# Performance work log

Measured on AMD Instinct MI355X. Metric: run time of the kernel, lower is better.

Reference implementation:

```python
import jax, jax.numpy as jnp
import numpy as np
import math

B, S, D, H = 4, 1024, 512, 8
DK = D // H
NEG = -1e32


def setup_inputs() -> dict:
    key = jax.random.key(0)
    ks = jax.random.split(key, 16)
    f = lambda k, shape: jax.random.normal(k, shape, dtype=jnp.float32)
    w = 1.0 / math.sqrt(D)  # xavier-ish scale
    return {
        'query_mean': f(ks[0], (B, S, D)),
        'query_cov': f(ks[1], (B, S, D)),
        'key_mean': f(ks[2], (B, S, D)),
        'key_cov': f(ks[3], (B, S, D)),
        'values_mean': f(ks[4], (B, S, D)),
        'values_cov': f(ks[5], (B, S, D)),
        'Wk_mean': f(ks[6], (D, D)) * w, 'bk_mean': jnp.zeros((D,), jnp.float32),
        'Wk_cov': f(ks[7], (D, D)) * w, 'bk_cov': jnp.zeros((D,), jnp.float32),
        'Wv_mean': f(ks[8], (D, D)) * w, 'bv_mean': jnp.zeros((D,), jnp.float32),
        'Wv_cov': f(ks[9], (D, D)) * w, 'bv_cov': jnp.zeros((D,), jnp.float32),
        'Wo_mean': f(ks[10], (D, D)) * w, 'bo_mean': jnp.zeros((D,), jnp.float32),
        'Wo_cov': f(ks[11], (D, D)) * w, 'bo_cov': jnp.zeros((D,), jnp.float32),
        'gammas': f(ks[12], (H, 1, 1)) * 0.1,
        'mask': jnp.tril(jnp.ones((1, 1, S, S), dtype=jnp.int32)),
    }


def _forward(query_mean, query_cov, key_mean, key_cov, values_mean, values_cov,
             Wk_mean, bk_mean, Wk_cov, bk_cov, Wv_mean, bv_mean, Wv_cov, bv_cov,
             Wo_mean, bo_mean, Wo_cov, bo_cov, gammas, mask):
    def heads(x, W, b):  # [B,S,D] -> [B,H,S,DK]
        return (x @ W + b).reshape(B, S, H, DK).transpose(0, 2, 1, 3)

    # kq_same=True: queries and keys share the k linears
    qm = heads(query_mean, Wk_mean, bk_mean)
    qc = heads(query_cov, Wk_cov, bk_cov)
    km = heads(key_mean, Wk_mean, bk_mean)
    kc = heads(key_cov, Wk_cov, bk_cov)
    vm = heads(values_mean, Wv_mean, bv_mean)
    vc = heads(values_cov, Wv_cov, bv_cov)

    inv = 1.0 / math.sqrt(DK)
    sm = jnp.einsum('bhqd,bhkd->bhqk', qm, km) * inv  # [B,H,S,S]
    sc = jnp.einsum('bhqd,bhkd->bhqk', qc, kc) * inv

    maskf = mask.astype(jnp.float32)
    # position_effect[i,j] = |j - i|
    pos = jnp.abs(jnp.arange(S)[None, :] - jnp.arange(S)[:, None]).astype(jnp.float32)[None, None]

    def dist_scores(s):
        p = jax.nn.softmax(jnp.where(mask == 0, NEG, s), axis=-1) * maskf
        cum = jnp.cumsum(p, axis=-1)
        tot = jnp.sum(p, axis=-1, keepdims=True)
        return jnp.sqrt(jnp.clip((tot - cum) * pos, 0.0, None))

    dm = jax.lax.stop_gradient(dist_scores(sm))  # torch no_grad + detach
    dc = jax.lax.stop_gradient(dist_scores(sc))

    gv = -jax.nn.softplus(gammas)[None]  # [1,H,1,1]
    em = jnp.clip(jnp.exp(dm * gv), 1e-5, 1e5)
    ec = jnp.clip(jnp.exp(dc * gv), 1e-5, 1e5)

    am = jax.nn.softmax(jnp.where(mask == 0, NEG, sm * em), axis=-1)
    ac = jax.nn.softmax(jnp.where(mask == 0, NEG, sc * ec), axis=-1)

    om = jnp.einsum('bhqk,bhkd->bhqd', am, vm).transpose(0, 2, 1, 3).reshape(B, S, D)
    oc = jnp.einsum('bhqk,bhkd->bhqd', ac, vc).transpose(0, 2, 1, 3).reshape(B, S, D)
    return om @ Wo_mean + bo_mean, oc @ Wo_cov + bo_cov


def reference(query_mean, query_cov, key_mean, key_cov, values_mean, values_cov,
              Wk_mean, bk_mean, Wk_cov, bk_cov, Wv_mean, bv_mean, Wv_cov, bv_cov,
              Wo_mean, bo_mean, Wo_cov, bo_cov, gammas, mask):
    return _forward(query_mean, query_cov, key_mean, key_cov, values_mean, values_cov,
                    Wk_mean, bk_mean, Wk_cov, bk_cov, Wv_mean, bv_mean, Wv_cov, bv_cov,
                    Wo_mean, bo_mean, Wo_cov, bo_cov, gammas, mask)
```

## Files before the change

### kernel.cpp

```cpp
#include <hip/hip_runtime.h>
#include <hip/hip_bf16.h>
#include <math.h>

constexpr int B_  = 4;
constexpr int S_  = 1024;
constexpr int D_  = 512;
constexpr int H_  = 8;
constexpr int DK_ = 64;
constexpr int MROWS_ = B_ * S_;
constexpr size_t SZ_ = (size_t)B_ * H_ * S_ * DK_;
constexpr size_t WSZ_ = (size_t)D_ * D_;

typedef __attribute__((ext_vector_type(8))) short bf16x8;
typedef __attribute__((ext_vector_type(4))) float f32x4;

__device__ __forceinline__ float bf2f(unsigned short u) {
  union { unsigned int u; float f; } v; v.u = (unsigned int)u << 16; return v.f;
}
__device__ __forceinline__ unsigned short f2bf(float f) {
  union { float f; unsigned int u; } v; v.f = f;
  unsigned int r = v.u + 0x7FFFu + ((v.u >> 16) & 1u);
  return (unsigned short)(r >> 16);
}
__device__ __forceinline__ unsigned short f2bf_ru(float f) {
  union { float f; unsigned int u; } v; v.f = f;
  return (unsigned short)((v.u + 0x8000u) >> 16);
}

template <int CTRL>
__device__ __forceinline__ float dpp_mov_f(float x) {
  return __builtin_bit_cast(float,
      __builtin_amdgcn_update_dpp(0, __builtin_bit_cast(int, x), CTRL, 0xF, 0xF, true));
}
__device__ __forceinline__ float scan16(float v) {
  v += dpp_mov_f<0x111>(v);
  v += dpp_mov_f<0x112>(v);
  v += dpp_mov_f<0x114>(v);
  v += dpp_mov_f<0x118>(v);
  return v;
}
__device__ __forceinline__ float red16(float v) {
  v += dpp_mov_f<0x128>(v);
  v += dpp_mov_f<0x124>(v);
  v += dpp_mov_f<0x122>(v);
  v += dpp_mov_f<0x121>(v);
  return v;
}
__device__ __forceinline__ float bcast15(float v) {
  return __builtin_bit_cast(float,
      __builtin_amdgcn_ds_swizzle(__builtin_bit_cast(int, v), 0x01F0));
}

struct TpArgs { const float* W[4]; unsigned short* out[4]; };

__global__ __launch_bounds__(256) void wtrans(TpArgs a) {
  const int z = blockIdx.z;
  const float* __restrict__ W = a.W[z];
  unsigned short* __restrict__ out = a.out[z];
  __shared__ float T[64][65];
  const int tid = threadIdx.x;
  const int tx = blockIdx.x & 7, ty = blockIdx.x >> 3;
  const int k0 = ty * 64, n0 = tx * 64;
#pragma unroll
  for (int i = 0; i < 4; ++i) {
    const int idx = tid + i * 256;
    const int r = idx >> 4, c4 = (idx & 15) * 4;
    const float4 w = *(const float4*)&W[(size_t)(k0 + r) * D_ + n0 + c4];
    T[r][c4 + 0] = w.x; T[r][c4 + 1] = w.y; T[r][c4 + 2] = w.z; T[r][c4 + 3] = w.w;
  }
  __syncthreads();
#pragma unroll
  for (int i = 0; i < 4; ++i) {
    const int idx = tid + i * 256;
    const int n = idx >> 4, kc = (idx & 15) * 4;
    ushort4 pk;
    pk.x = f2bf(T[kc + 0][n]); pk.y = f2bf(T[kc + 1][n]);
    pk.z = f2bf(T[kc + 2][n]); pk.w = f2bf(T[kc + 3][n]);
    *(ushort4*)&out[(size_t)(n0 + n) * D_ + k0 + kc] = pk;
  }
}

struct ProjArgs {
  const float* A[6]; const unsigned short* Wt[6]; const float* bias[6];
  unsigned short* out[6]; int vmode[6];
};

__global__ __launch_bounds__(256) void proj_mfma(ProjArgs args) {
  const int z = blockIdx.z;
  const float* __restrict__ A = args.A[z];
  const unsigned short* __restrict__ Wt = args.Wt[z];
  const float* __restrict__ bias = args.bias[z];
  unsigned short* __restrict__ out = args.out[z];
  const int vmode = args.vmode[z];

  __shared__ unsigned short Abuf[128][40];
  __shared__ unsigned short Bbuf[128][40];
  const int tid = threadIdx.x, wv = tid >> 6, lane = tid & 63;
  const int quad = lane >> 4, l16 = lane & 15;
  const int wm = wv >> 1, wn = wv & 1;
  const int n0 = blockIdx.x * 128, m0 = blockIdx.y * 128;

  f32x4 acc[4][4];
#pragma unroll
  for (int i = 0; i < 4; ++i)
#pragma unroll
    for (int j = 0; j < 4; ++j) acc[i][j] = (f32x4){0.f, 0.f, 0.f, 0.f};

  for (int kt = 0; kt < 16; ++kt) {
    const int k0 = kt * 32;
    __syncthreads();
#pragma unroll
    for (int i = 0; i < 4; ++i) {
      const int idx = tid + i * 256;
      const int m = idx >> 3, c = idx & 7;
      const float4 av = *(const float4*)&A[(size_t)(m0 + m) * D_ + k0 + c * 4];
      ushort4 p;
      p.x = f2bf(av.x); p.y = f2bf(av.y); p.z = f2bf(av.z); p.w = f2bf(av.w);
      *(ushort4*)&Abuf[m][c * 4] = p;
    }
#pragma unroll
    for (int i = 0; i < 2; ++i) {
      const int idx = tid + i * 256;
      const int n = idx >> 2, c = idx & 3;
      *(uint4*)&Bbuf[n][c * 8] = *(const uint4*)&Wt[(size_t)(n0 + n) * D_ + k0 + c * 8];
    }
    __syncthreads();

    bf16x8 af[4], bfr[4];
#pragma unroll
    for (int i = 0; i < 4; ++i) af[i] = *(const bf16x8*)&Abuf[wm * 64 + i * 16 + l16][quad * 8];
#pragma unroll
    for (int j = 0; j < 4; ++j) bfr[j] = *(const bf16x8*)&Bbuf[wn * 64 + j * 16 + l16][quad * 8];
#pragma unroll
    for (int i = 0; i < 4; ++i)
#pragma unroll
      for (int j = 0; j < 4; ++j)
        acc[i][j] = __builtin_amdgcn_mfma_f32_16x16x32_bf16(af[i], bfr[j], acc[i][j], 0, 0, 0);
  }

#pragma unroll
  for (int j = 0; j < 4; ++j) {
    const int col = n0 + wn * 64 + j * 16 + l16;
    const float bv = bias[col];
    const int h = col >> 6, dk = col & 63;
#pragma unroll
    for (int i = 0; i < 4; ++i) {
      const int mbase = m0 + wm * 64 + i * 16 + quad * 4;
      const int b = mbase >> 10;
      if (!vmode) {
#pragma unroll
        for (int r = 0; r < 4; ++r) {
          const int s = (mbase + r) & 1023;
          out[(((size_t)b * H_ + h) * S_ + s) * DK_ + dk] = f2bf(acc[i][j][r] + bv);
        }
      } else {
        const int s = mbase & 1023;
        ushort4 pk;
        pk.x = f2bf(acc[i][j][0] + bv); pk.y = f2bf(acc[i][j][1] + bv);
        pk.z = f2bf(acc[i][j][2] + bv); pk.w = f2bf(acc[i][j][3] + bv);
        *(ushort4*)&out[(((size_t)b * H_ + h) * DK_ + dk) * S_ + s] = pk;
      }
    }
  }
}

struct OutArgs {
  const unsigned short* A[2]; const unsigned short* Wt[2];
  const float* bias[2]; float* out[2];
};

__global__ __launch_bounds__(256) void out_mfma(OutArgs args) {
  const int z = blockIdx.z;
  const unsigned short* __restrict__ A = args.A[z];
  const unsigned short* __restrict__ Wt = args.Wt[z];
  const float* __restrict__ bias = args.bias[z];
  float* __restrict__ out = args.out[z];

  __shared__ unsigned short Abuf[128][40];
  __shared__ unsigned short Bbuf[128][40];
  const int tid = threadIdx.x, wv = tid >> 6, lane = tid & 63;
  const int quad = lane >> 4, l16 = lane & 15;
  const int wm = wv >> 1, wn = wv & 1;
  const int n0 = blockIdx.x * 128, m0 = blockIdx.y * 128;

  f32x4 acc[4][4];
#pragma unroll
  for (int i = 0; i < 4; ++i)
#pragma unroll
    for (int j = 0; j < 4; ++j) acc[i][j] = (f32x4){0.f, 0.f, 0.f, 0.f};

  for (int kt = 0; kt < 16; ++kt) {
    const int k0 = kt * 32;
    __syncthreads();
#pragma unroll
    for (int i = 0; i < 2; ++i) {
      const int idx = tid + i * 256;
      const int m = idx >> 2, c = idx & 3;
      *(uint4*)&Abuf[m][c * 8] = *(const uint4*)&A[(size_t)(m0 + m) * D_ + k0 + c * 8];
    }
#pragma unroll
    for (int i = 0; i < 2; ++i) {
      const int idx = tid + i * 256;
      const int n = idx >> 2, c = idx & 3;
      *(uint4*)&Bbuf[n][c * 8] = *(const uint4*)&Wt[(size_t)(n0 + n) * D_ + k0 + c * 8];
    }
    __syncthreads();

    bf16x8 af[4], bfr[4];
#pragma unroll
    for (int i = 0; i < 4; ++i) af[i] = *(const bf16x8*)&Abuf[wm * 64 + i * 16 + l16][quad * 8];
#pragma unroll
    for (int j = 0; j < 4; ++j) bfr[j] = *(const bf16x8*)&Bbuf[wn * 64 + j * 16 + l16][quad * 8];
#pragma unroll
    for (int i = 0; i < 4; ++i)
#pragma unroll
      for (int j = 0; j < 4; ++j)
        acc[i][j] = __builtin_amdgcn_mfma_f32_16x16x32_bf16(af[i], bfr[j], acc[i][j], 0, 0, 0);
  }

#pragma unroll
  for (int j = 0; j < 4; ++j) {
    const int col = n0 + wn * 64 + j * 16 + l16;
    const float bv = bias[col];
#pragma unroll
    for (int i = 0; i < 4; ++i) {
      const int mbase = m0 + wm * 64 + i * 16 + quad * 4;
#pragma unroll
      for (int r = 0; r < 4; ++r)
        out[(size_t)(mbase + r) * D_ + col] = acc[i][j][r] + bv;
    }
  }
}

__global__ __launch_bounds__(256) void attn_mfma(
    const unsigned short* __restrict__ qkv, const float* __restrict__ gammas,
    unsigned short* __restrict__ Obase)
{
  __shared__ unsigned short Ps[4][16][72];

  const int tid = threadIdx.x;
  const int w = tid >> 6, lane = tid & 63, quad = lane >> 4, l16 = lane & 15;
  const int bh = blockIdx.x;
  const int qt = 15 - (int)blockIdx.y;
  const int ch = blockIdx.z;
  const int wq = w;
  const int q0 = qt << 6;
  const int b = bh >> 3, h = bh & 7;

  constexpr float SC_ = 0.125f * 1.4426950408889634f;
  constexpr float LOG2E_ = 1.4426950408889634f;

  const unsigned short* Q  = qkv + (size_t)ch * 3 * SZ_ + (size_t)bh * S_ * DK_;
  const unsigned short* K  = qkv + (size_t)ch * 3 * SZ_ + SZ_ + (size_t)bh * S_ * DK_;
  const unsigned short* Vt = qkv + (size_t)ch * 3 * SZ_ + 2 * SZ_ + (size_t)bh * (size_t)DK_ * S_;
  unsigned short* O = Obase + (size_t)ch * SZ_;

  const float g = gammas[h];
  const float gv2 = -(fmaxf(g, 0.f) + log1pf(__expf(-fabsf(g)))) * LOG2E_;

  const unsigned short* Qrow = Q + (size_t)(q0 + wq * 16 + l16) * DK_;
  const bf16x8 qf0 = *(const bf16x8*)(Qrow + quad * 8);
  const bf16x8 qf1 = *(const bf16x8*)(Qrow + 32 + quad * 8);
  const int myrow = q0 + wq * 16 + quad * 4;

  float Tacc[4] = {0.f, 0.f, 0.f, 0.f};
  for (int kt = 0; kt <= qt; ++kt) {
    f32x4 sa[4];
#pragma unroll
    for (int cb = 0; cb < 4; ++cb) {
      const unsigned short* Kr = K + (size_t)(kt * 64 + cb * 16 + l16) * DK_;
      const bf16x8 kf0 = *(const bf16x8*)(Kr + quad * 8);
      const bf16x8 kf1 = *(const bf16x8*)(Kr + 32 + quad * 8);
      f32x4 a = {0.f, 0.f, 0.f, 0.f};
      a = __builtin_amdgcn_mfma_f32_16x16x32_bf16(qf0, kf0, a, 0, 0, 0);
      a = __builtin_amdgcn_mfma_f32_16x16x32_bf16(qf1, kf1, a, 0, 0, 0);
      sa[cb] = a;
    }
    if (kt == qt) {
#pragma unroll
      for (int cb = 0; cb < 4; ++cb)
#pragma unroll
        for (int r = 0; r < 4; ++r) {
          float e = exp2f(sa[cb][r] * SC_);
          if ((kt * 64 + cb * 16 + l16) > (myrow + r)) e = 0.f;
          Tacc[r] += e;
        }
    } else {
#pragma unroll
      for (int cb = 0; cb < 4; ++cb)
#pragma unroll
        for (int r = 0; r < 4; ++r)
          Tacc[r] += exp2f(sa[cb][r] * SC_);
    }
  }
  float invT[4];
#pragma unroll
  for (int r = 0; r < 4; ++r) invT[r] = 1.f / red16(Tacc[r]);

  float carry[4] = {0.f, 0.f, 0.f, 0.f};
  float l2a[4] = {0.f, 0.f, 0.f, 0.f};
  f32x4 oacc[4];
#pragma unroll
  for (int cb = 0; cb < 4; ++cb) oacc[cb] = (f32x4){0.f, 0.f, 0.f, 0.f};

  for (int kt = 0; kt <= qt; ++kt) {
    bf16x8 vf0[4], vf1[4];
#pragma unroll
    for (int cb = 0; cb < 4; ++cb) {
      const unsigned short* Vr = Vt + (size_t)(cb * 16 + l16) * S_ + kt * 64;
      vf0[cb] = *(const bf16x8*)(Vr + quad * 8);
      vf1[cb] = *(const bf16x8*)(Vr + 32 + quad * 8);
    }

    f32x4 sa[4];
#pragma unroll
    for (int cb = 0; cb < 4; ++cb) {
      const unsigned short* Kr = K + (size_t)(kt * 64 + cb * 16 + l16) * DK_;
      const bf16x8 kf0 = *(const bf16x8*)(Kr + quad * 8);
      const bf16x8 kf1 = *(const bf16x8*)(Kr + 32 + quad * 8);
      f32x4 a = {0.f, 0.f, 0.f, 0.f};
      a = __builtin_amdgcn_mfma_f32_16x16x32_bf16(qf0, kf0, a, 0, 0, 0);
      a = __builtin_amdgcn_mfma_f32_16x16x32_bf16(qf1, kf1, a, 0, 0, 0);
      sa[cb] = a;
    }
#pragma unroll
    for (int cb = 0; cb < 4; ++cb)
#pragma unroll
      for (int r = 0; r < 4; ++r) sa[cb][r] *= SC_;
    if (kt == qt) {
#pragma unroll
      for (int cb = 0; cb < 4; ++cb)
#pragma unroll
        for (int r = 0; r < 4; ++r)
          if ((kt * 64 + cb * 16 + l16) > (myrow + r)) sa[cb][r] = -1e30f;
    }

#pragma unroll
    for (int r = 0; r < 4; ++r) {
      float v0 = scan16(exp2f(sa[0][r]));
      float v1 = scan16(exp2f(sa[1][r]));
      float v2 = scan16(exp2f(sa[2][r]));
      float v3 = scan16(exp2f(sa[3][r]));
      const float tt0 = bcast15(v0), tt1 = bcast15(v1);
      const float tt2 = bcast15(v2), tt3 = bcast15(v3);
      const float base = carry[r];
      const float p01 = tt0 + tt1, p012 = p01 + tt2;
      const float cum0 = (base + v0) * invT[r];
      const float cum1 = (base + tt0 + v1) * invT[r];
      const float cum2 = (base + p01 + v2) * invT[r];
      const float cum3 = (base + p012 + v3) * invT[r];
      carry[r] = base + p012 + tt3;

      const float bpos = (float)(myrow + r) - (float)(kt * 64 + l16);
      float st0, st1, st2, st3;
      {
        float dd = sqrtf(fmaxf((1.f - cum0) * bpos, 0.f));
        st0 = sa[0][r] * fminf(fmaxf(exp2f(dd * gv2), 1e-5f), 1e5f);
        dd = sqrtf(fmaxf((1.f - cum1) * (bpos - 16.f), 0.f));
        st1 = sa[1][r] * fminf(fmaxf(exp2f(dd * gv2), 1e-5f), 1e5f);
        dd = sqrtf(fmaxf((1.f - cum2) * (bpos - 32.f), 0.f));
        st2 = sa[2][r] * fminf(fmaxf(exp2f(dd * gv2), 1e-5f), 1e5f);
        dd = sqrtf(fmaxf((1.f - cum3) * (bpos - 48.f), 0.f));
        st3 = sa[3][r] * fminf(fmaxf(exp2f(dd * gv2), 1e-5f), 1e5f);
      }

      const float w0 = exp2f(st0), w1 = exp2f(st1);
      const float w2 = exp2f(st2), w3 = exp2f(st3);
      l2a[r] += (w0 + w1) + (w2 + w3);
      const int prow = quad * 4 + r;
      Ps[w][prow][ 0 + l16] = f2bf_ru(w0);
      Ps[w][prow][16 + l16] = f2bf_ru(w1);
      Ps[w][prow][32 + l16] = f2bf_ru(w2);
      Ps[w][prow][48 + l16] = f2bf_ru(w3);
    }
    asm volatile("s_waitcnt lgkmcnt(0)" ::: "memory");

    const bf16x8 pf0 = *(const bf16x8*)&Ps[w][l16][quad * 8];
    const bf16x8 pf1 = *(const bf16x8*)&Ps[w][l16][32 + quad * 8];
#pragma unroll
    for (int cb = 0; cb < 4; ++cb) {
      oacc[cb] = __builtin_amdgcn_mfma_f32_16x16x32_bf16(pf0, vf0[cb], oacc[cb], 0, 0, 0);
      oacc[cb] = __builtin_amdgcn_mfma_f32_16x16x32_bf16(pf1, vf1[cb], oacc[cb], 0, 0, 0);
    }
  }

#pragma unroll
  for (int r = 0; r < 4; ++r) {
    const float inv = 1.f / red16(l2a[r]);
    const int srow = myrow + r;
    const size_t base = ((size_t)b * S_ + srow) * D_ + h * DK_;
    O[base +  0 + l16] = f2bf(oacc[0][r] * inv);
    O[base + 16 + l16] = f2bf(oacc[1][r] * inv);
    O[base + 32 + l16] = f2bf(oacc[2][r] * inv);
    O[base + 48 + l16] = f2bf(oacc[3][r] * inv);
  }
}

extern "C" void kernel_launch(void* const* d_in, const int* in_sizes, int n_in,
                              void* d_out, int out_size, void* d_ws, size_t ws_size,
                              hipStream_t stream) {
  const float* query_mean  = (const float*)d_in[0];
  const float* query_cov   = (const float*)d_in[1];
  const float* key_mean    = (const float*)d_in[2];
  const float* key_cov     = (const float*)d_in[3];
  const float* values_mean = (const float*)d_in[4];
  const float* values_cov  = (const float*)d_in[5];
  const float* Wk_mean = (const float*)d_in[6];
  const float* bk_mean = (const float*)d_in[7];
  const float* Wk_cov  = (const float*)d_in[8];
  const float* bk_cov  = (const float*)d_in[9];
  const float* Wv_mean = (const float*)d_in[10];
  const float* bv_mean = (const float*)d_in[11];
  const float* Wv_cov  = (const float*)d_in[12];
  const float* bv_cov  = (const float*)d_in[13];
  const float* Wo_mean = (const float*)d_in[14];
  const float* bo_mean = (const float*)d_in[15];
  const float* Wo_cov  = (const float*)d_in[16];
  const float* bo_cov  = (const float*)d_in[17];
  const float* gammas  = (const float*)d_in[18];

  unsigned short* qkv  = (unsigned short*)d_ws;
  unsigned short* obuf = qkv + 6 * SZ_;
  unsigned short* Wt4  = (unsigned short*)d_out;
  unsigned short* Wot  = qkv + 2 * SZ_;
  float* out = (float*)d_out;

  TpArgs t1;
  t1.W[0] = Wk_mean; t1.W[1] = Wv_mean; t1.W[2] = Wk_cov; t1.W[3] = Wv_cov;
  for (int i = 0; i < 4; ++i) t1.out[i] = Wt4 + (size_t)i * WSZ_;
  wtrans<<<dim3(64, 1, 4), 256, 0, stream>>>(t1);

  ProjArgs pa;
  const float* pA[6] = {query_mean, key_mean, values_mean, query_cov, key_cov, values_cov};
  const int   wIdx[6] = {0, 0, 1, 2, 2, 3};
  const float* pb[6] = {bk_mean, bk_mean, bv_mean, bk_cov, bk_cov, bv_cov};
  const int pv[6] = {0, 0, 1, 0, 0, 1};
  for (int i = 0; i < 6; ++i) {
    pa.A[i] = pA[i]; pa.Wt[i] = Wt4 + (size_t)wIdx[i] * WSZ_; pa.bias[i] = pb[i];
    pa.out[i] = qkv + (size_t)i * SZ_; pa.vmode[i] = pv[i];
  }
  proj_mfma<<<dim3(4, 32, 6), 256, 0, stream>>>(pa);

  attn_mfma<<<dim3(32, 16, 2), 256, 0, stream>>>(qkv, gammas, obuf);

  TpArgs t2;
  t2.W[0] = Wo_mean; t2.W[1] = Wo_cov; t2.W[2] = Wo_mean; t2.W[3] = Wo_cov;
  t2.out[0] = Wot; t2.out[1] = Wot + WSZ_; t2.out[2] = Wot; t2.out[3] = Wot + WSZ_;
  wtrans<<<dim3(64, 1, 2), 256, 0, stream>>>(t2);

  OutArgs oa;
  oa.A[0] = obuf;        oa.A[1] = obuf + SZ_;
  oa.Wt[0] = Wot;        oa.Wt[1] = Wot + WSZ_;
  oa.bias[0] = bo_mean;  oa.bias[1] = bo_cov;
  oa.out[0] = out;       oa.out[1] = out + (size_t)MROWS_ * D_;
  out_mfma<<<dim3(4, 32, 2), 256, 0, stream>>>(oa);
}
```

Before: 289.1 us.

## Pair causal query tiles per block and software-pipeline K loads in attention

The attention kernel now uses 512-thread blocks that pair a long causal query tile with a short one, which balances per-block work and halves the grid. The first pass processes two K tiles per iteration, and the main pass prefetches the next K tile and issues its QK MFMA while the current tile is still being processed. V loads are moved later in the loop. Segment totals now come from a DPP reduction instead of a ds_swizzle broadcast, and the redundant upper clamp on the decay factor is dropped. Costs are higher register pressure under launch_bounds(512,4), and waves within a block that do unequal amounts of work.

```diff
diff --git a/kernel.cpp b/kernel.cpp
--- a/kernel.cpp
+++ b/kernel.cpp
@@ -45,10 +45,6 @@
   v += dpp_mov_f<0x122>(v);
   v += dpp_mov_f<0x121>(v);
   return v;
-}
-__device__ __forceinline__ float bcast15(float v) {
-  return __builtin_bit_cast(float,
-      __builtin_amdgcn_ds_swizzle(__builtin_bit_cast(int, v), 0x01F0));
 }
 
 struct TpArgs { const float* W[4]; unsigned short* out[4]; };
@@ -232,18 +228,19 @@
   }
 }
 
-__global__ __launch_bounds__(256) void attn_mfma(
+__global__ __launch_bounds__(512, 4) void attn_mfma(
     const unsigned short* __restrict__ qkv, const float* __restrict__ gammas,
     unsigned short* __restrict__ Obase)
 {
-  __shared__ unsigned short Ps[4][16][72];
+  __shared__ unsigned short Ps[8][16][72];
 
   const int tid = threadIdx.x;
   const int w = tid >> 6, lane = tid & 63, quad = lane >> 4, l16 = lane & 15;
   const int bh = blockIdx.x;
-  const int qt = 15 - (int)blockIdx.y;
+  const int pair = blockIdx.y;
   const int ch = blockIdx.z;
-  const int wq = w;
+  const int qt = (w < 4) ? (15 - pair) : pair;
+  const int wq = w & 3;
   const int q0 = qt << 6;
   const int b = bh >> 3, h = bh & 7;
 
@@ -263,26 +260,51 @@
   const bf16x8 qf1 = *(const bf16x8*)(Qrow + 32 + quad * 8);
   const int myrow = q0 + wq * 16 + quad * 4;
 
-  float Tacc[4] = {0.f, 0.f, 0.f, 0.f};
-  for (int kt = 0; kt <= qt; ++kt) {
-    f32x4 sa[4];
+  auto loadK = [&](int kt, bf16x8 (&kf)[8]) {
 #pragma unroll
     for (int cb = 0; cb < 4; ++cb) {
       const unsigned short* Kr = K + (size_t)(kt * 64 + cb * 16 + l16) * DK_;
-      const bf16x8 kf0 = *(const bf16x8*)(Kr + quad * 8);
-      const bf16x8 kf1 = *(const bf16x8*)(Kr + 32 + quad * 8);
+      kf[2 * cb]     = *(const bf16x8*)(Kr + quad * 8);
+      kf[2 * cb + 1] = *(const bf16x8*)(Kr + 32 + quad * 8);
+    }
+  };
+  auto qk = [&](const bf16x8 (&kf)[8], f32x4 (&sa)[4]) {
+#pragma unroll
+    for (int cb = 0; cb < 4; ++cb) {
       f32x4 a = {0.f, 0.f, 0.f, 0.f};
-      a = __builtin_amdgcn_mfma_f32_16x16x32_bf16(qf0, kf0, a, 0, 0, 0);
-      a = __builtin_amdgcn_mfma_f32_16x16x32_bf16(qf1, kf1, a, 0, 0, 0);
+      a = __builtin_amdgcn_mfma_f32_16x16x32_bf16(qf0, kf[2 * cb], a, 0, 0, 0);
+      a = __builtin_amdgcn_mfma_f32_16x16x32_bf16(qf1, kf[2 * cb + 1], a, 0, 0, 0);
       sa[cb] = a;
     }
-    if (kt == qt) {
+  };
+
+  float Tacc[4] = {0.f, 0.f, 0.f, 0.f};
+  int ka = 0;
+  for (; ka + 1 < qt; ka += 2) {
+    bf16x8 kfa[8], kfb[8];
+    loadK(ka, kfa);
+    loadK(ka + 1, kfb);
+    f32x4 s1[4], s2[4];
+    qk(kfa, s1);
+    qk(kfb, s2);
+#pragma unroll
+    for (int cb = 0; cb < 4; ++cb)
+#pragma unroll
+      for (int r = 0; r < 4; ++r)
+        Tacc[r] += exp2f(s1[cb][r] * SC_) + exp2f(s2[cb][r] * SC_);
+  }
+  for (; ka <= qt; ++ka) {
+    bf16x8 kfa[8];
+    loadK(ka, kfa);
+    f32x4 s1[4];
+    qk(kfa, s1);
+    if (ka == qt) {
 #pragma unroll
       for (int cb = 0; cb < 4; ++cb)
 #pragma unroll
         for (int r = 0; r < 4; ++r) {
-          float e = exp2f(sa[cb][r] * SC_);
-          if ((kt * 64 + cb * 16 + l16) > (myrow + r)) e = 0.f;
+          float e = exp2f(s1[cb][r] * SC_);
+          if ((ka * 64 + cb * 16 + l16) > (myrow + r)) e = 0.f;
           Tacc[r] += e;
         }
     } else {
@@ -290,7 +312,7 @@
       for (int cb = 0; cb < 4; ++cb)
 #pragma unroll
         for (int r = 0; r < 4; ++r)
-          Tacc[r] += exp2f(sa[cb][r] * SC_);
+          Tacc[r] += exp2f(s1[cb][r] * SC_);
     }
   }
   float invT[4];
@@ -303,66 +325,55 @@
 #pragma unroll
   for (int cb = 0; cb < 4; ++cb) oacc[cb] = (f32x4){0.f, 0.f, 0.f, 0.f};
 
-  for (int kt = 0; kt <= qt; ++kt) {
-    bf16x8 vf0[4], vf1[4];
-#pragma unroll
-    for (int cb = 0; cb < 4; ++cb) {
-      const unsigned short* Vr = Vt + (size_t)(cb * 16 + l16) * S_ + kt * 64;
-      vf0[cb] = *(const bf16x8*)(Vr + quad * 8);
-      vf1[cb] = *(const bf16x8*)(Vr + 32 + quad * 8);
-    }
-
-    f32x4 sa[4];
-#pragma unroll
-    for (int cb = 0; cb < 4; ++cb) {
-      const unsigned short* Kr = K + (size_t)(kt * 64 + cb * 16 + l16) * DK_;
-      const bf16x8 kf0 = *(const bf16x8*)(Kr + quad * 8);
-      const bf16x8 kf1 = *(const bf16x8*)(Kr + 32 + quad * 8);
-      f32x4 a = {0.f, 0.f, 0.f, 0.f};
-      a = __builtin_amdgcn_mfma_f32_16x16x32_bf16(qf0, kf0, a, 0, 0, 0);
-      a = __builtin_amdgcn_mfma_f32_16x16x32_bf16(qf1, kf1, a, 0, 0, 0);
-      sa[cb] = a;
-    }
+  f32x4 sa[4];
+  {
+    bf16x8 kf0_[8];
+    loadK(0, kf0_);
+    qk(kf0_, sa);
+  }
+
+  for (int t = 0; t <= qt; ++t) {
+    bf16x8 kfn[8];
+    if (t < qt) loadK(t + 1, kfn);
+
 #pragma unroll
     for (int cb = 0; cb < 4; ++cb)
 #pragma unroll
       for (int r = 0; r < 4; ++r) sa[cb][r] *= SC_;
-    if (kt == qt) {
+    if (t == qt) {
 #pragma unroll
       for (int cb = 0; cb < 4; ++cb)
 #pragma unroll
         for (int r = 0; r < 4; ++r)
-          if ((kt * 64 + cb * 16 + l16) > (myrow + r)) sa[cb][r] = -1e30f;
+          if ((t * 64 + cb * 16 + l16) > (myrow + r)) sa[cb][r] = -1e30f;
     }
 
 #pragma unroll
     for (int r = 0; r < 4; ++r) {
-      float v0 = scan16(exp2f(sa[0][r]));
-      float v1 = scan16(exp2f(sa[1][r]));
-      float v2 = scan16(exp2f(sa[2][r]));
-      float v3 = scan16(exp2f(sa[3][r]));
-      const float tt0 = bcast15(v0), tt1 = bcast15(v1);
-      const float tt2 = bcast15(v2), tt3 = bcast15(v3);
+      const float e0 = exp2f(sa[0][r]), e1 = exp2f(sa[1][r]);
+      const float e2 = exp2f(sa[2][r]), e3 = exp2f(sa[3][r]);
+      const float v0 = scan16(e0), v1 = scan16(e1);
+      const float v2 = scan16(e2), v3 = scan16(e3);
+      const float t0 = red16(e0), t1 = red16(e1);
+      const float t2 = red16(e2), t3 = red16(e3);
       const float base = carry[r];
-      const float p01 = tt0 + tt1, p012 = p01 + tt2;
+      const float p01 = t0 + t1, p012 = p01 + t2;
       const float cum0 = (base + v0) * invT[r];
-      const float cum1 = (base + tt0 + v1) * invT[r];
+      const float cum1 = (base + t0 + v1) * invT[r];
       const float cum2 = (base + p01 + v2) * invT[r];
       const float cum3 = (base + p012 + v3) * invT[r];
-      carry[r] = base + p012 + tt3;
-
-      const float bpos = (float)(myrow + r) - (float)(kt * 64 + l16);
-      float st0, st1, st2, st3;
-      {
-        float dd = sqrtf(fmaxf((1.f - cum0) * bpos, 0.f));
-        st0 = sa[0][r] * fminf(fmaxf(exp2f(dd * gv2), 1e-5f), 1e5f);
-        dd = sqrtf(fmaxf((1.f - cum1) * (bpos - 16.f), 0.f));
-        st1 = sa[1][r] * fminf(fmaxf(exp2f(dd * gv2), 1e-5f), 1e5f);
-        dd = sqrtf(fmaxf((1.f - cum2) * (bpos - 32.f), 0.f));
-        st2 = sa[2][r] * fminf(fmaxf(exp2f(dd * gv2), 1e-5f), 1e5f);
-        dd = sqrtf(fmaxf((1.f - cum3) * (bpos - 48.f), 0.f));
-        st3 = sa[3][r] * fminf(fmaxf(exp2f(dd * gv2), 1e-5f), 1e5f);
-      }
+      carry[r] = base + p012 + t3;
+
+      const float bpos = (float)(myrow + r) - (float)(t * 64 + l16);
+      float dd, st0, st1, st2, st3;
+      dd = sqrtf(fmaxf((1.f - cum0) * bpos, 0.f));
+      st0 = sa[0][r] * fmaxf(exp2f(dd * gv2), 1e-5f);
+      dd = sqrtf(fmaxf((1.f - cum1) * (bpos - 16.f), 0.f));
+      st1 = sa[1][r] * fmaxf(exp2f(dd * gv2), 1e-5f);
+      dd = sqrtf(fmaxf((1.f - cum2) * (bpos - 32.f), 0.f));
+      st2 = sa[2][r] * fmaxf(exp2f(dd * gv2), 1e-5f);
+      dd = sqrtf(fmaxf((1.f - cum3) * (bpos - 48.f), 0.f));
+      st3 = sa[3][r] * fmaxf(exp2f(dd * gv2), 1e-5f);
 
       const float w0 = exp2f(st0), w1 = exp2f(st1);
       const float w2 = exp2f(st2), w3 = exp2f(st3);
@@ -373,10 +384,21 @@
       Ps[w][prow][32 + l16] = f2bf_ru(w2);
       Ps[w][prow][48 + l16] = f2bf_ru(w3);
     }
+
+    bf16x8 vf0[4], vf1[4];
+#pragma unroll
+    for (int cb = 0; cb < 4; ++cb) {
+      const unsigned short* Vr = Vt + (size_t)(cb * 16 + l16) * S_ + t * 64;
+      vf0[cb] = *(const bf16x8*)(Vr + quad * 8);
+      vf1[cb] = *(const bf16x8*)(Vr + 32 + quad * 8);
+    }
+
     asm volatile("s_waitcnt lgkmcnt(0)" ::: "memory");
-
     const bf16x8 pf0 = *(const bf16x8*)&Ps[w][l16][quad * 8];
     const bf16x8 pf1 = *(const bf16x8*)&Ps[w][l16][32 + quad * 8];
+
+    if (t < qt) qk(kfn, sa);
+
 #pragma unroll
     for (int cb = 0; cb < 4; ++cb) {
       oacc[cb] = __builtin_amdgcn_mfma_f32_16x16x32_bf16(pf0, vf0[cb], oacc[cb], 0, 0, 0);
@@ -441,7 +463,7 @@
   }
   proj_mfma<<<dim3(4, 32, 6), 256, 0, stream>>>(pa);
 
-  attn_mfma<<<dim3(32, 16, 2), 256, 0, stream>>>(qkv, gammas, obuf);
+  attn_mfma<<<dim3(32, 8, 2), 512, 0, stream>>>(qkv, gammas, obuf);
 
   TpArgs t2;
   t2.W[0] = Wo_mean; t2.W[1] = Wo_cov; t2.W[2] = Wo_mean; t2.W[3] = Wo_cov;
```

New measurement: 362.7 us. +25.5%, slower.

## Pair causal query tiles per block, add MFMA priority hints, trim softmax math

Applied to the files above, without the earlier changes.

Each attention block now runs 512 threads and handles two query tiles, a long one (15-pair) and a short one (pair), so causal work is balanced across blocks and the grid is halved. MFMA sections are wrapped in s_setprio to favour matrix issue when waves interleave. The per-16-lane tile totals are now computed with a DPP reduction instead of a ds_swizzle broadcast, and the upper 1e5 clamp is dropped because exp of a non-positive argument cannot exceed 1. This trades a larger block with more registers per CU for better load balance across blocks.

```diff
diff --git a/kernel.cpp b/kernel.cpp
--- a/kernel.cpp
+++ b/kernel.cpp
@@ -45,10 +45,6 @@
   v += dpp_mov_f<0x122>(v);
   v += dpp_mov_f<0x121>(v);
   return v;
-}
-__device__ __forceinline__ float bcast15(float v) {
-  return __builtin_bit_cast(float,
-      __builtin_amdgcn_ds_swizzle(__builtin_bit_cast(int, v), 0x01F0));
 }
 
 struct TpArgs { const float* W[4]; unsigned short* out[4]; };
@@ -232,18 +228,19 @@
   }
 }
 
-__global__ __launch_bounds__(256) void attn_mfma(
+__global__ __launch_bounds__(512) void attn_mfma(
     const unsigned short* __restrict__ qkv, const float* __restrict__ gammas,
     unsigned short* __restrict__ Obase)
 {
-  __shared__ unsigned short Ps[4][16][72];
+  __shared__ unsigned short Ps[8][16][72];
 
   const int tid = threadIdx.x;
   const int w = tid >> 6, lane = tid & 63, quad = lane >> 4, l16 = lane & 15;
   const int bh = blockIdx.x;
-  const int qt = 15 - (int)blockIdx.y;
+  const int pair = blockIdx.y;
   const int ch = blockIdx.z;
-  const int wq = w;
+  const int qt = (w < 4) ? (15 - pair) : pair;
+  const int wq = w & 3;
   const int q0 = qt << 6;
   const int b = bh >> 3, h = bh & 7;
 
@@ -266,6 +263,7 @@
   float Tacc[4] = {0.f, 0.f, 0.f, 0.f};
   for (int kt = 0; kt <= qt; ++kt) {
     f32x4 sa[4];
+    __builtin_amdgcn_s_setprio(1);
 #pragma unroll
     for (int cb = 0; cb < 4; ++cb) {
       const unsigned short* Kr = K + (size_t)(kt * 64 + cb * 16 + l16) * DK_;
@@ -276,6 +274,7 @@
       a = __builtin_amdgcn_mfma_f32_16x16x32_bf16(qf1, kf1, a, 0, 0, 0);
       sa[cb] = a;
     }
+    __builtin_amdgcn_s_setprio(0);
     if (kt == qt) {
 #pragma unroll
       for (int cb = 0; cb < 4; ++cb)
@@ -313,6 +312,7 @@
     }
 
     f32x4 sa[4];
+    __builtin_amdgcn_s_setprio(1);
 #pragma unroll
     for (int cb = 0; cb < 4; ++cb) {
       const unsigned short* Kr = K + (size_t)(kt * 64 + cb * 16 + l16) * DK_;
@@ -323,6 +323,7 @@
       a = __builtin_amdgcn_mfma_f32_16x16x32_bf16(qf1, kf1, a, 0, 0, 0);
       sa[cb] = a;
     }
+    __builtin_amdgcn_s_setprio(0);
 #pragma unroll
     for (int cb = 0; cb < 4; ++cb)
 #pragma unroll
@@ -337,32 +338,30 @@
 
 #pragma unroll
     for (int r = 0; r < 4; ++r) {
-      float v0 = scan16(exp2f(sa[0][r]));
-      float v1 = scan16(exp2f(sa[1][r]));
-      float v2 = scan16(exp2f(sa[2][r]));
-      float v3 = scan16(exp2f(sa[3][r]));
-      const float tt0 = bcast15(v0), tt1 = bcast15(v1);
-      const float tt2 = bcast15(v2), tt3 = bcast15(v3);
+      const float e0 = exp2f(sa[0][r]), e1 = exp2f(sa[1][r]);
+      const float e2 = exp2f(sa[2][r]), e3 = exp2f(sa[3][r]);
+      const float v0 = scan16(e0), v1 = scan16(e1);
+      const float v2 = scan16(e2), v3 = scan16(e3);
+      const float t0 = red16(e0), t1 = red16(e1);
+      const float t2 = red16(e2), t3 = red16(e3);
       const float base = carry[r];
-      const float p01 = tt0 + tt1, p012 = p01 + tt2;
+      const float p01 = t0 + t1, p012 = p01 + t2;
       const float cum0 = (base + v0) * invT[r];
-      const float cum1 = (base + tt0 + v1) * invT[r];
+      const float cum1 = (base + t0 + v1) * invT[r];
       const float cum2 = (base + p01 + v2) * invT[r];
       const float cum3 = (base + p012 + v3) * invT[r];
-      carry[r] = base + p012 + tt3;
+      carry[r] = base + p012 + t3;
 
       const float bpos = (float)(myrow + r) - (float)(kt * 64 + l16);
-      float st0, st1, st2, st3;
-      {
-        float dd = sqrtf(fmaxf((1.f - cum0) * bpos, 0.f));
-        st0 = sa[0][r] * fminf(fmaxf(exp2f(dd * gv2), 1e-5f), 1e5f);
-        dd = sqrtf(fmaxf((1.f - cum1) * (bpos - 16.f), 0.f));
-        st1 = sa[1][r] * fminf(fmaxf(exp2f(dd * gv2), 1e-5f), 1e5f);
-        dd = sqrtf(fmaxf((1.f - cum2) * (bpos - 32.f), 0.f));
-        st2 = sa[2][r] * fminf(fmaxf(exp2f(dd * gv2), 1e-5f), 1e5f);
-        dd = sqrtf(fmaxf((1.f - cum3) * (bpos - 48.f), 0.f));
-        st3 = sa[3][r] * fminf(fmaxf(exp2f(dd * gv2), 1e-5f), 1e5f);
-      }
+      float dd, st0, st1, st2, st3;
+      dd = sqrtf(fmaxf((1.f - cum0) * bpos, 0.f));
+      st0 = sa[0][r] * fmaxf(exp2f(dd * gv2), 1e-5f);
+      dd = sqrtf(fmaxf((1.f - cum1) * (bpos - 16.f), 0.f));
+      st1 = sa[1][r] * fmaxf(exp2f(dd * gv2), 1e-5f);
+      dd = sqrtf(fmaxf((1.f - cum2) * (bpos - 32.f), 0.f));
+      st2 = sa[2][r] * fmaxf(exp2f(dd * gv2), 1e-5f);
+      dd = sqrtf(fmaxf((1.f - cum3) * (bpos - 48.f), 0.f));
+      st3 = sa[3][r] * fmaxf(exp2f(dd * gv2), 1e-5f);
 
       const float w0 = exp2f(st0), w1 = exp2f(st1);
       const float w2 = exp2f(st2), w3 = exp2f(st3);
@@ -377,11 +376,13 @@
 
     const bf16x8 pf0 = *(const bf16x8*)&Ps[w][l16][quad * 8];
     const bf16x8 pf1 = *(const bf16x8*)&Ps[w][l16][32 + quad * 8];
+    __builtin_amdgcn_s_setprio(1);
 #pragma unroll
     for (int cb = 0; cb < 4; ++cb) {
       oacc[cb] = __builtin_amdgcn_mfma_f32_16x16x32_bf16(pf0, vf0[cb], oacc[cb], 0, 0, 0);
       oacc[cb] = __builtin_amdgcn_mfma_f32_16x16x32_bf16(pf1, vf1[cb], oacc[cb], 0, 0, 0);
     }
+    __builtin_amdgcn_s_setprio(0);
   }
 
 #pragma unroll
@@ -441,7 +442,7 @@
   }
   proj_mfma<<<dim3(4, 32, 6), 256, 0, stream>>>(pa);
 
-  attn_mfma<<<dim3(32, 16, 2), 256, 0, stream>>>(qkv, gammas, obuf);
+  attn_mfma<<<dim3(32, 8, 2), 512, 0, stream>>>(qkv, gammas, obuf);
 
   TpArgs t2;
   t2.W[0] = Wo_mean; t2.W[1] = Wo_cov; t2.W[2] = Wo_mean; t2.W[3] = Wo_cov;
```

Result: no change. 290.7 us (+0.6%).

## Pair causal query tiles per block and use raw hardware exp/sqrt/rcp

Applied to the files above, without the earlier changes.

The attention kernel now launches 512-thread blocks, each covering two query tiles (qt and 15-qt), so every block gets the same amount of causal work. This removes the load imbalance from the triangular mask and halves the grid. It also swaps exp2f, sqrtf and division for raw v_exp/v_sqrt/v_rcp intrinsics and drops the redundant upper 1e5 clamp, which cuts instruction count at some accuracy cost. The larger blocks may lower occupancy through register pressure.

```diff
diff --git a/kernel.cpp b/kernel.cpp
--- a/kernel.cpp
+++ b/kernel.cpp
@@ -25,6 +25,28 @@
 __device__ __forceinline__ unsigned short f2bf_ru(float f) {
   union { float f; unsigned int u; } v; v.f = f;
   return (unsigned short)((v.u + 0x8000u) >> 16);
+}
+
+__device__ __forceinline__ float ex2(float x) {
+#if __has_builtin(__builtin_amdgcn_exp2f)
+  return __builtin_amdgcn_exp2f(x);
+#else
+  float r; asm("v_exp_f32 %0, %1" : "=v"(r) : "v"(x)); return r;
+#endif
+}
+__device__ __forceinline__ float fsqrt_raw(float x) {
+#if __has_builtin(__builtin_amdgcn_sqrtf)
+  return __builtin_amdgcn_sqrtf(x);
+#else
+  float r; asm("v_sqrt_f32 %0, %1" : "=v"(r) : "v"(x)); return r;
+#endif
+}
+__device__ __forceinline__ float frcp_raw(float x) {
+#if __has_builtin(__builtin_amdgcn_rcpf)
+  return __builtin_amdgcn_rcpf(x);
+#else
+  float r; asm("v_rcp_f32 %0, %1" : "=v"(r) : "v"(x)); return r;
+#endif
 }
 
 template <int CTRL>
@@ -232,18 +254,19 @@
   }
 }
 
-__global__ __launch_bounds__(256) void attn_mfma(
+__global__ __launch_bounds__(512) void attn_mfma(
     const unsigned short* __restrict__ qkv, const float* __restrict__ gammas,
     unsigned short* __restrict__ Obase)
 {
-  __shared__ unsigned short Ps[4][16][72];
+  __shared__ unsigned short Ps[8][16][72];
 
   const int tid = threadIdx.x;
   const int w = tid >> 6, lane = tid & 63, quad = lane >> 4, l16 = lane & 15;
   const int bh = blockIdx.x;
-  const int qt = 15 - (int)blockIdx.y;
+  const int pair = blockIdx.y;
   const int ch = blockIdx.z;
-  const int wq = w;
+  const int qt = (w < 4) ? (15 - pair) : pair;
+  const int wq = w & 3;
   const int q0 = qt << 6;
   const int b = bh >> 3, h = bh & 7;
 
@@ -281,7 +304,7 @@
       for (int cb = 0; cb < 4; ++cb)
 #pragma unroll
         for (int r = 0; r < 4; ++r) {
-          float e = exp2f(sa[cb][r] * SC_);
+          float e = ex2(sa[cb][r] * SC_);
           if ((kt * 64 + cb * 16 + l16) > (myrow + r)) e = 0.f;
           Tacc[r] += e;
         }
@@ -290,12 +313,12 @@
       for (int cb = 0; cb < 4; ++cb)
 #pragma unroll
         for (int r = 0; r < 4; ++r)
-          Tacc[r] += exp2f(sa[cb][r] * SC_);
+          Tacc[r] += ex2(sa[cb][r] * SC_);
     }
   }
   float invT[4];
 #pragma unroll
-  for (int r = 0; r < 4; ++r) invT[r] = 1.f / red16(Tacc[r]);
+  for (int r = 0; r < 4; ++r) invT[r] = frcp_raw(red16(Tacc[r]));
 
   float carry[4] = {0.f, 0.f, 0.f, 0.f};
   float l2a[4] = {0.f, 0.f, 0.f, 0.f};
@@ -337,10 +360,10 @@
 
 #pragma unroll
     for (int r = 0; r < 4; ++r) {
-      float v0 = scan16(exp2f(sa[0][r]));
-      float v1 = scan16(exp2f(sa[1][r]));
-      float v2 = scan16(exp2f(sa[2][r]));
-      float v3 = scan16(exp2f(sa[3][r]));
+      float v0 = scan16(ex2(sa[0][r]));
+      float v1 = scan16(ex2(sa[1][r]));
+      float v2 = scan16(ex2(sa[2][r]));
+      float v3 = scan16(ex2(sa[3][r]));
       const float tt0 = bcast15(v0), tt1 = bcast15(v1);
       const float tt2 = bcast15(v2), tt3 = bcast15(v3);
       const float base = carry[r];
@@ -352,20 +375,18 @@
       carry[r] = base + p012 + tt3;
 
       const float bpos = (float)(myrow + r) - (float)(kt * 64 + l16);
-      float st0, st1, st2, st3;
-      {
-        float dd = sqrtf(fmaxf((1.f - cum0) * bpos, 0.f));
-        st0 = sa[0][r] * fminf(fmaxf(exp2f(dd * gv2), 1e-5f), 1e5f);
-        dd = sqrtf(fmaxf((1.f - cum1) * (bpos - 16.f), 0.f));
-        st1 = sa[1][r] * fminf(fmaxf(exp2f(dd * gv2), 1e-5f), 1e5f);
-        dd = sqrtf(fmaxf((1.f - cum2) * (bpos - 32.f), 0.f));
-        st2 = sa[2][r] * fminf(fmaxf(exp2f(dd * gv2), 1e-5f), 1e5f);
-        dd = sqrtf(fmaxf((1.f - cum3) * (bpos - 48.f), 0.f));
-        st3 = sa[3][r] * fminf(fmaxf(exp2f(dd * gv2), 1e-5f), 1e5f);
-      }
-
-      const float w0 = exp2f(st0), w1 = exp2f(st1);
-      const float w2 = exp2f(st2), w3 = exp2f(st3);
+      float dd, st0, st1, st2, st3;
+      dd = fsqrt_raw(fmaxf((1.f - cum0) * bpos, 0.f));
+      st0 = sa[0][r] * fmaxf(ex2(dd * gv2), 1e-5f);
+      dd = fsqrt_raw(fmaxf((1.f - cum1) * (bpos - 16.f), 0.f));
+      st1 = sa[1][r] * fmaxf(ex2(dd * gv2), 1e-5f);
+      dd = fsqrt_raw(fmaxf((1.f - cum2) * (bpos - 32.f), 0.f));
+      st2 = sa[2][r] * fmaxf(ex2(dd * gv2), 1e-5f);
+      dd = fsqrt_raw(fmaxf((1.f - cum3) * (bpos - 48.f), 0.f));
+      st3 = sa[3][r] * fmaxf(ex2(dd * gv2), 1e-5f);
+
+      const float w0 = ex2(st0), w1 = ex2(st1);
+      const float w2 = ex2(st2), w3 = ex2(st3);
       l2a[r] += (w0 + w1) + (w2 + w3);
       const int prow = quad * 4 + r;
       Ps[w][prow][ 0 + l16] = f2bf_ru(w0);
@@ -386,7 +407,7 @@
 
 #pragma unroll
   for (int r = 0; r < 4; ++r) {
-    const float inv = 1.f / red16(l2a[r]);
+    const float inv = frcp_raw(red16(l2a[r]));
     const int srow = myrow + r;
     const size_t base = ((size_t)b * S_ + srow) * D_ + h * DK_;
     O[base +  0 + l16] = f2bf(oacc[0][r] * inv);
@@ -441,7 +462,7 @@
   }
   proj_mfma<<<dim3(4, 32, 6), 256, 0, stream>>>(pa);
 
-  attn_mfma<<<dim3(32, 16, 2), 256, 0, stream>>>(qkv, gammas, obuf);
+  attn_mfma<<<dim3(32, 8, 2), 512, 0, stream>>>(qkv, gammas, obuf);
 
   TpArgs t2;
   t2.W[0] = Wo_mean; t2.W[1] = Wo_cov; t2.W[2] = Wo_mean; t2.W[3] = Wo_cov;
```

Result: faster. 267.6 us (-7.4%).
